# Optimization experiments

Hardware: AMD Instinct MI355X
Metric: run time of the kernel (lower is better)

## Reference

```python
import jax, jax.numpy as jnp
import numpy as np

V, D, H, L, RATIO, T_MAX = 1024, 512, 8, 11, 3, 1024
DH = D // H
HID = D * RATIO
NB, DB = 2048, 128  # bigram buckets / dim
EPS = 1e-6


def _rope_tables(T):
    pos = jnp.arange(T, dtype=jnp.float32)
    freqs = 1.0 / (10000.0 ** (jnp.arange(0, DH, 2, dtype=jnp.float32) / DH))
    emb = jnp.outer(pos, freqs)  # [T, DH/2]
    return jnp.cos(emb), jnp.sin(emb)


def _rmsnorm(x, w):
    return x * jax.lax.rsqrt(jnp.mean(x * x, axis=-1, keepdims=True) + EPS) * w


def setup_inputs() -> dict:
    key = jax.random.key(0)
    ks = jax.random.split(key, 10)
    B, T = 8, 1024
    s = 0.02
    return {
        "x": jax.random.randint(ks[0], (B, T), 0, V),
        "embed": jax.random.normal(ks[1], (V, D), jnp.float32) * s,
        "Wqkv": jax.random.normal(ks[2], (L, 3 * D, D), jnp.float32) * s,
        "Wproj": jax.random.normal(ks[3], (L, D, D), jnp.float32) * s,
        "n1_w": jnp.ones((L, D), jnp.float32),
        "n2_w": jnp.ones((L, D), jnp.float32),
        "Wfc1": jax.random.normal(ks[4], (L, HID, D), jnp.float32) * s,
        "Wfc2": jax.random.normal(ks[5], (L, D, HID), jnp.float32) * s,
        "norm_f_w": jnp.ones((D,), jnp.float32),
        "bg_embed": jax.random.normal(ks[6], (NB, DB), jnp.float32) * s,
        "bg_proj": jax.random.normal(ks[7], (V, DB), jnp.float32) * s,
    }


def _attn(x, Wqkv, Wproj, cos, sin, causal):
    B, T, C = x.shape
    qkv = x @ Wqkv.T  # [B,T,3D]
    q, k, v = jnp.split(qkv, 3, axis=-1)
    def heads(t):
        return t.reshape(B, T, H, DH).transpose(0, 2, 1, 3)  # [B,H,T,DH]
    q, k, v = heads(q), heads(k), heads(v)
    c = cos[None, None]  # [1,1,T,DH/2]
    s = sin[None, None]
    def rope(t):
        t1, t2 = t[..., : DH // 2], t[..., DH // 2 :]
        return jnp.concatenate([t1 * c - t2 * s, t1 * s + t2 * c], axis=-1)
    q, k = rope(q), rope(k)
    w = jnp.einsum("bhqd,bhkd->bhqk", q, k) * (DH ** -0.5)
    w = jnp.where(causal, w, -jnp.inf)
    w = jax.nn.softmax(w.astype(jnp.float32), axis=-1).astype(x.dtype)
    out = jnp.einsum("bhqk,bhkd->bhqd", w, v)
    self_w = jnp.diagonal(w, axis1=-2, axis2=-1)[..., None]  # [B,H,T,1]
    out = out - self_w * v  # XSA: subtract self-value contribution
    out = out.transpose(0, 2, 1, 3).reshape(B, T, C)
    return out @ Wproj.T


def reference(x, embed, Wqkv, Wproj, n1_w, n2_w, Wfc1, Wfc2, norm_f_w, bg_embed, bg_proj):
    B, T = x.shape
    cos, sin = _rope_tables(T_MAX)
    cos, sin = cos[:T], sin[:T]
    causal = jnp.tril(jnp.ones((T, T), dtype=bool))
    # bigram logits from previous token
    prev = jnp.concatenate([jnp.zeros((B, 1), x.dtype), x[:, :-1]], axis=1)
    bigram_logits = bg_embed[prev % NB] @ bg_proj.T  # [B,T,V]
    h = embed[x]
    for i in range(L):
        h = h + _attn(_rmsnorm(h, n1_w[i]), Wqkv[i], Wproj[i], cos, sin, causal)
        z = _rmsnorm(h, n2_w[i])
        h = h + jnp.square(jax.nn.relu(z @ Wfc1[i].T)) @ Wfc2[i].T
    h = _rmsnorm(h, norm_f_w)
    return h @ embed.T + bigram_logits
```

## Files before the change

### kernel.cpp

```cpp
#include <hip/hip_runtime.h>

#define NROW   8192
#define DMODEL 512
#define TSEQ   1024
#define LAYERS 11
#define HIDDEN 1536

typedef __bf16 bf16_t;
typedef bf16_t bf16x8 __attribute__((ext_vector_type(8)));
typedef bf16_t bf16x4 __attribute__((ext_vector_type(4)));
typedef float  f32x4  __attribute__((ext_vector_type(4)));
typedef unsigned int u32;
typedef u32 u32x4 __attribute__((ext_vector_type(4)));

#define GLD16(gp, lp) __builtin_amdgcn_global_load_lds( \
    (const __attribute__((address_space(1))) void*)(gp), \
    (__attribute__((address_space(3))) void*)(lp), 16, 0, 0)

#if __has_builtin(__builtin_amdgcn_exp2f)
#define EXP2(x) __builtin_amdgcn_exp2f(x)
#else
#define EXP2(x) exp2f(x)
#endif

__global__ void rope_table_k(float* __restrict__ cosT, float* __restrict__ sinT) {
    int i = blockIdx.x * blockDim.x + threadIdx.x;
    int t = i >> 5, j = i & 31;
    float freq = powf(10000.f, -(float)j * (1.f / 32.f));
    float ang = (float)t * freq;
    cosT[i] = cosf(ang);
    sinT[i] = sinf(ang);
}

__global__ void embed_gather_k(const int* __restrict__ x,
                               const float* __restrict__ embed,
                               float* __restrict__ h,
                               bf16_t* __restrict__ hb) {
    int n = blockIdx.x;
    int d = threadIdx.x;
    float4 v = ((const float4*)(embed + (size_t)x[n] * DMODEL))[d];
    ((float4*)(h + (size_t)n * DMODEL))[d] = v;
    bf16x4 o;
    o[0] = (bf16_t)v.x; o[1] = (bf16_t)v.y; o[2] = (bf16_t)v.z; o[3] = (bf16_t)v.w;
    *(bf16x4*)(hb + (size_t)n * DMODEL + d * 4) = o;
}

__global__ void bg_gather_k(const int* __restrict__ x,
                            const float* __restrict__ bge,
                            bf16_t* __restrict__ Afu) {
    int n = blockIdx.x;
    int t = n & (TSEQ - 1);
    int prev = (t == 0) ? 0 : x[n - 1];
    Afu[(size_t)n * 640 + 512 + threadIdx.x] = (bf16_t)bge[(size_t)prev * 128 + threadIdx.x];
}

__global__ void cvt_bf16_k(const float* __restrict__ in, bf16_t* __restrict__ out, int n8) {
    int i = blockIdx.x * blockDim.x + threadIdx.x;
    if (i >= n8) return;
    float4 a = ((const float4*)in)[2 * i];
    float4 b = ((const float4*)in)[2 * i + 1];
    bf16x8 o;
    o[0] = (bf16_t)a.x; o[1] = (bf16_t)a.y; o[2] = (bf16_t)a.z; o[3] = (bf16_t)a.w;
    o[4] = (bf16_t)b.x; o[5] = (bf16_t)b.y; o[6] = (bf16_t)b.z; o[7] = (bf16_t)b.w;
    ((bf16x8*)out)[i] = o;
}

__global__ void cvt_fold_k(const float* __restrict__ in,
                           const float* __restrict__ nw,
                           bf16_t* __restrict__ out, int n8, int layerSz) {
    int i = blockIdx.x * blockDim.x + threadIdx.x;
    if (i >= n8) return;
    int i8 = i * 8;
    int k = i8 & 511;
    int l = i8 / layerSz;
    const float* wv = nw + l * DMODEL + k;
    float4 a = ((const float4*)in)[2 * i];
    float4 b = ((const float4*)in)[2 * i + 1];
    float4 wa = *(const float4*)wv;
    float4 wb = *(const float4*)(wv + 4);
    bf16x8 o;
    o[0] = (bf16_t)(a.x * wa.x); o[1] = (bf16_t)(a.y * wa.y);
    o[2] = (bf16_t)(a.z * wa.z); o[3] = (bf16_t)(a.w * wa.w);
    o[4] = (bf16_t)(b.x * wb.x); o[5] = (bf16_t)(b.y * wb.y);
    o[6] = (bf16_t)(b.z * wb.z); o[7] = (bf16_t)(b.w * wb.w);
    ((bf16x8*)out)[i] = o;
}

__global__ void cvt_pad_k(const float* __restrict__ in, bf16_t* __restrict__ out,
                          int n8, int lshift, int mask, int colOff) {
    int i = blockIdx.x * blockDim.x + threadIdx.x;
    if (i >= n8) return;
    int i8 = i * 8;
    int row = i8 >> lshift;
    int col = i8 & mask;
    float4 a = ((const float4*)in)[2 * i];
    float4 b = ((const float4*)in)[2 * i + 1];
    bf16x8 o;
    o[0] = (bf16_t)a.x; o[1] = (bf16_t)a.y; o[2] = (bf16_t)a.z; o[3] = (bf16_t)a.w;
    o[4] = (bf16_t)b.x; o[5] = (bf16_t)b.y; o[6] = (bf16_t)b.z; o[7] = (bf16_t)b.w;
    *(bf16x8*)&out[(size_t)row * 640 + colOff + col] = o;
}

__global__ __launch_bounds__(256) void rmsnorm_k(const float* __restrict__ in,
                                                 const float* __restrict__ w,
                                                 bf16_t* __restrict__ out,
                                                 int ostride) {
    int wv = threadIdx.x >> 6, lane = threadIdx.x & 63;
    int row = (blockIdx.x << 2) + wv;
    const float* rp = in + (size_t)row * DMODEL + lane * 8;
    float4 v0 = *(const float4*)(rp);
    float4 v1 = *(const float4*)(rp + 4);
    float ss = v0.x*v0.x + v0.y*v0.y + v0.z*v0.z + v0.w*v0.w
             + v1.x*v1.x + v1.y*v1.y + v1.z*v1.z + v1.w*v1.w;
#pragma unroll
    for (int off = 32; off; off >>= 1) ss += __shfl_xor(ss, off, 64);
    float sc = rsqrtf(ss * (1.f / DMODEL) + 1e-6f);
    const float* wp = w + lane * 8;
    float4 w0 = *(const float4*)(wp);
    float4 w1 = *(const float4*)(wp + 4);
    bf16x8 o;
    o[0] = (bf16_t)(v0.x * sc * w0.x); o[1] = (bf16_t)(v0.y * sc * w0.y);
    o[2] = (bf16_t)(v0.z * sc * w0.z); o[3] = (bf16_t)(v0.w * sc * w0.w);
    o[4] = (bf16_t)(v1.x * sc * w1.x); o[5] = (bf16_t)(v1.y * sc * w1.y);
    o[6] = (bf16_t)(v1.z * sc * w1.z); o[7] = (bf16_t)(v1.w * sc * w1.w);
    *(bf16x8*)(out + (size_t)row * ostride + lane * 8) = o;
}

template<int BM, int EPI>
__global__ __launch_bounds__(256, 2)
void gemm_mfma(const bf16_t* __restrict__ A,
               const bf16_t* __restrict__ B,
               float* __restrict__ Cf,
               bf16_t* __restrict__ Cb,
               const float* __restrict__ cosT,
               const float* __restrict__ sinT,
               int M, int N, int K, int nbx) {
    constexpr int NT  = 256;
    constexpr int WM  = 2;
    constexpr int MI  = BM / WM / 16;
    constexpr int ACH = (BM * 4) / NT;
    constexpr int BCH = 2;
    constexpr int NBUF = (BM == 64) ? 4 : 3;
    constexpr bool SCALED = (EPI == 2 || EPI == 4);
    __shared__ __align__(16) bf16_t As[NBUF][BM * 32];
    __shared__ __align__(16) bf16_t Bs[NBUF][128 * 32];
    const int tid = threadIdx.x;
    const int w = tid >> 6, lane = tid & 63;

    const int nwg = (int)gridDim.x;
    const int bid = blockIdx.x;
    const int swz = (bid & 7) * (nwg >> 3) + (bid >> 3);
    const int bx = swz % nbx, by = swz / nbx;

    const int m0 = by * BM, n0 = bx * 128;
    const int wr = (w >> 1) * (BM / WM), wc = (w & 1) * 64;
    const int fr = lane & 15, fq = lane >> 4;

    f32x4 acc[MI][4] = {};
    float ssq[SCALED ? MI : 1] = {};

    float cold[EPI == 1 ? MI : 1][4][4];
    if constexpr (EPI == 1) {
#pragma unroll
        for (int i = 0; i < MI; ++i)
#pragma unroll
            for (int j = 0; j < 4; ++j)
#pragma unroll
                for (int q = 0; q < 4; ++q)
                    cold[i][j][q] = Cf[(size_t)(m0 + wr + i * 16 + fq * 4 + q) * N
                                       + n0 + wc + j * 16 + fr];
    }

    auto stage = [&](int k0, int buf) {
#pragma unroll
        for (int c = 0; c < ACH; ++c) {
            int idx = c * NT + tid;
            int row = idx >> 2, cs = idx & 3;
            GLD16(A + (size_t)(m0 + row) * K + k0 + cs * 8,
                  &As[buf][(size_t)(c * NT + w * 64) * 8]);
        }
#pragma unroll
        for (int c = 0; c < BCH; ++c) {
            int idx = c * NT + tid;
            int row = idx >> 2, cs = idx & 3;
            GLD16(B + (size_t)(n0 + row) * K + k0 + cs * 8,
                  &Bs[buf][(size_t)(c * NT + w * 64) * 8]);
        }
    };

    const int NK = K >> 5;
    stage(0, 0);
    stage(32, 1);
    for (int k = 0; k < NK; ++k) {
        const int cur = k % NBUF;
        if (k + 2 < NK) {
            stage((k + 2) << 5, (k + 2) % NBUF);
            if constexpr (BM == 128) asm volatile("s_waitcnt vmcnt(8)" ::: "memory");
            else                     asm volatile("s_waitcnt vmcnt(6)" ::: "memory");
        } else if (k + 1 < NK) {
            if constexpr (BM == 128) asm volatile("s_waitcnt vmcnt(4)" ::: "memory");
            else                     asm volatile("s_waitcnt vmcnt(3)" ::: "memory");
        } else {
            asm volatile("s_waitcnt vmcnt(0)" ::: "memory");
        }
        __builtin_amdgcn_s_barrier();
        __builtin_amdgcn_sched_barrier(0);

        bf16x8 a[MI], b[4];
        const bf16_t* ap = &As[cur][(size_t)(wr + fr) * 32 + fq * 8];
        const bf16_t* bp = &Bs[cur][(size_t)(wc + fr) * 32 + fq * 8];
#pragma unroll
        for (int i = 0; i < MI; ++i) a[i] = *(const bf16x8*)(ap + i * 16 * 32);
#pragma unroll
        for (int j = 0; j < 4; ++j)  b[j] = *(const bf16x8*)(bp + j * 16 * 32);
        __builtin_amdgcn_s_setprio(1);
#pragma unroll
        for (int i = 0; i < MI; ++i)
#pragma unroll
            for (int j = 0; j < 4; ++j)
                acc[i][j] = __builtin_amdgcn_mfma_f32_16x16x32_bf16(a[i], b[j], acc[i][j], 0, 0, 0);
        __builtin_amdgcn_s_setprio(0);

        if constexpr (SCALED) {
#pragma unroll
            for (int i = 0; i < MI; ++i)
#pragma unroll
                for (int j = 0; j < 8; ++j) {
                    float f = (float)a[i][j];
                    ssq[i] = fmaf(f, f, ssq[i]);
                }
        }

        if constexpr (NBUF == 3) {
            asm volatile("s_waitcnt lgkmcnt(0)" ::: "memory");
            __builtin_amdgcn_s_barrier();
            __builtin_amdgcn_sched_barrier(0);
        }
    }

    float sld[SCALED ? MI : 1][4];
    if constexpr (SCALED) {
#pragma unroll
        for (int i = 0; i < MI; ++i) {
            ssq[i] += __shfl_xor(ssq[i], 16, 64);
            ssq[i] += __shfl_xor(ssq[i], 32, 64);
#pragma unroll
            for (int q = 0; q < 4; ++q) {
                float v = __shfl(ssq[i], fq * 4 + q, 64);
                sld[i][q] = rsqrtf(v * (1.f / DMODEL) + 1e-6f);
            }
        }
    }

    if (EPI == 4) {
        const bool qk = (n0 + wc) < 1024;
#pragma unroll
        for (int i = 0; i < MI; ++i) {
#pragma unroll
            for (int q = 0; q < 4; ++q) {
                int row = m0 + wr + i * 16 + fq * 4 + q;
                size_t rb = (size_t)row * N + n0 + wc;
                float sm = sld[i][q];
                if (qk) {
                    int t = row & (TSEQ - 1);
#pragma unroll
                    for (int j = 0; j < 2; ++j) {
                        int d = j * 16 + fr;
                        float c = cosT[t * 32 + d];
                        float s = sinT[t * 32 + d];
                        float v1 = acc[i][j][q] * sm, v2 = acc[i][j + 2][q] * sm;
                        Cb[rb + j * 16 + fr]       = (bf16_t)(v1 * c - v2 * s);
                        Cb[rb + (j + 2) * 16 + fr] = (bf16_t)(v1 * s + v2 * c);
                    }
                } else {
#pragma unroll
                    for (int j = 0; j < 4; ++j)
                        Cb[rb + j * 16 + fr] = (bf16_t)(acc[i][j][q] * sm);
                }
            }
        }
        return;
    }
#pragma unroll
    for (int i = 0; i < MI; ++i) {
        int row = m0 + wr + i * 16 + fq * 4;
#pragma unroll
        for (int j = 0; j < 4; ++j) {
            int col = n0 + wc + j * 16 + fr;
#pragma unroll
            for (int q = 0; q < 4; ++q) {
                float v = acc[i][j][q];
                size_t off = (size_t)(row + q) * N + col;
                if (EPI == 0)      Cf[off] = v;
                else if (EPI == 1) {
                    float nv = cold[i][j][q] + v;
                    Cf[off] = nv;
                    Cb[off] = (bf16_t)nv;
                } else if (EPI == 2) {
                    v = fmaxf(v * sld[i][q], 0.f);
                    Cb[off] = (bf16_t)(v * v);
                }
            }
        }
    }
}

__global__ __launch_bounds__(512) void attn_mfma_k(const bf16_t* __restrict__ qkvb,
                                                   bf16_t* __restrict__ outb) {
    __shared__ __align__(16) bf16_t Ks[2][64 * 64];
    __shared__ __align__(16) bf16_t VsT[2][2 * 64 * 32];

    const int tid = threadIdx.x;
    const int w  = tid >> 6;
    const int ln = tid & 63;
    const int lr = ln & 15;
    const int lg = ln >> 4;

    const int bid = blockIdx.x;
    const int p  = 7 - (bid >> 6);
    const int bh = bid & 63;
    const int b = bh >> 3, h = bh & 7;
    const int lastT = (p << 7) + 64;
    const int tq0  = (p << 7) + w * 16;
    const int qrow = tq0 + lr;
    const int wlast = tq0 & ~63;

    const bf16_t* Qg = qkvb + (size_t)b * TSEQ * 1536 + h * 64;
    const bf16_t* Kg = Qg + 512;
    const bf16_t* Vg = Qg + 1024;

    const int mk = tid >> 4;
    const int md = tid & 15;
    const int src0 = lr + 32 * (lg & 1);
    const int fsel = lg >> 1;
    const int gofs = 8 * (lg ^ ((lr >> 2) & 3));

    auto KSTAGE = [&](int t0, int buf) {
        int key = w * 8 + (ln >> 3);
        int dc  = (ln & 7) ^ (ln >> 3);
        GLD16(Kg + (size_t)(t0 + key) * 1536 + dc * 8, &Ks[buf][w * 512]);
    };
    auto VLOAD = [&](int t0, bf16x4* rv) {
#pragma unroll
        for (int i = 0; i < 4; ++i)
            rv[i] = *(const bf16x4*)(Vg + (size_t)(t0 + mk * 4 + i) * 1536 + md * 4);
    };
    auto VWRITE = [&](const bf16x4* rv, int buf) {
        const int s = mk >> 3;
#pragma unroll
        for (int jj = 0; jj < 4; ++jj) {
            int row = md * 4 + jj;
            bf16x4 wv;
            wv[0] = rv[0][jj]; wv[1] = rv[1][jj]; wv[2] = rv[2][jj]; wv[3] = rv[3][jj];
            int gx = (mk & 7) ^ ((md & 3) << 1);
            *(bf16x4*)&VsT[buf][s * 2048 + row * 32 + gx * 4] = wv;
        }
    };

    bf16x8 qreg[2];
    {
        const float QS = 0.1803368801f;
        const bf16_t* qp = Qg + (size_t)qrow * 1536 + lg * 8;
        qreg[0] = *(const bf16x8*)qp;
        qreg[1] = *(const bf16x8*)(qp + 32);
#pragma unroll
        for (int jj = 0; jj < 8; ++jj) {
            qreg[0][jj] = (bf16_t)((float)qreg[0][jj] * QS);
            qreg[1][jj] = (bf16_t)((float)qreg[1][jj] * QS);
        }
    }

    f32x4 accO[4] = {};
    float mrun = -1e30f, pl = 0.f, esf = 0.f;

    {
        bf16x4 rv[4];
        KSTAGE(0, 0);
        if (w < 4) VLOAD(0, rv);
        asm volatile("s_waitcnt vmcnt(0)" ::: "memory");
        if (w < 4) VWRITE(rv, 0);
        asm volatile("s_waitcnt lgkmcnt(0)" ::: "memory");
        __builtin_amdgcn_s_barrier();
        __builtin_amdgcn_sched_barrier(0);
    }

    for (int t0 = 0; t0 <= lastT; t0 += 64) {
        const int cur = (t0 >> 6) & 1;
        const bool more = t0 < lastT;
        bf16x4 rv[4];
        if (more) {
            KSTAGE(t0 + 64, cur ^ 1);
            if (w < 4) VLOAD(t0 + 64, rv);
        }

        if (t0 <= wlast) {
            const bool masked = t0 == wlast;

            f32x4 sq[4] = {};
            __builtin_amdgcn_s_setprio(1);
#pragma unroll
            for (int kr = 0; kr < 4; ++kr) {
                int key = kr * 16 + lr;
#pragma unroll
                for (int s = 0; s < 2; ++s) {
                    int chunk = key * 8 + ((s * 4 + lg) ^ (key & 7));
                    bf16x8 kf = *(const bf16x8*)&Ks[cur][chunk * 8];
                    sq[kr] = __builtin_amdgcn_mfma_f32_16x16x32_bf16(kf, qreg[s], sq[kr], 0, 0, 0);
                }
            }
            __builtin_amdgcn_s_setprio(0);

            float e16[4][4];
            float tm = -1e30f;
            if (masked) {
#pragma unroll
                for (int f = 0; f < 4; ++f)
#pragma unroll
                    for (int r = 0; r < 4; ++r) {
                        int key = t0 + f * 16 + lg * 4 + r;
                        float sv = (key <= qrow) ? sq[f][r] : -1e30f;
                        e16[f][r] = sv;
                        tm = fmaxf(tm, sv);
                    }
            } else {
#pragma unroll
                for (int f = 0; f < 4; ++f)
#pragma unroll
                    for (int r = 0; r < 4; ++r) {
                        e16[f][r] = sq[f][r];
                        tm = fmaxf(tm, sq[f][r]);
                    }
            }
            tm = fmaxf(tm, __shfl_xor(tm, 16, 64));
            tm = fmaxf(tm, __shfl_xor(tm, 32, 64));

            const bool resc = __any(tm > mrun + 8.f);
            float mnew = resc ? fmaxf(mrun, tm) : mrun;
            float psum = 0.f;
#pragma unroll
            for (int f = 0; f < 4; ++f)
#pragma unroll
                for (int r = 0; r < 4; ++r) {
                    float e = EXP2(e16[f][r] - mnew);
                    e16[f][r] = e;
                    psum += e;
                }
            float pd = 0.f;
            if (masked) {
#pragma unroll
                for (int f = 0; f < 4; ++f)
#pragma unroll
                    for (int r = 0; r < 4; ++r) {
                        int key = t0 + f * 16 + lg * 4 + r;
                        pd = (key == qrow) ? e16[f][r] : pd;
                    }
            }
            if (resc) {
                float corr = EXP2(mrun - mnew);
                mrun = mnew;
                pl  = pl  * corr + psum;
                esf = esf * corr + pd;
#pragma unroll
                for (int dblk = 0; dblk < 4; ++dblk)
#pragma unroll
                    for (int r = 0; r < 4; ++r) accO[dblk][r] *= corr;
            } else {
                pl  += psum;
                esf += pd;
            }

            u32 plo[4], phi[4];
#pragma unroll
            for (int f = 0; f < 4; ++f) {
                bf16x4 t;
                t[0] = (bf16_t)e16[f][0]; t[1] = (bf16_t)e16[f][1];
                t[2] = (bf16_t)e16[f][2]; t[3] = (bf16_t)e16[f][3];
                uint2 pr = __builtin_bit_cast(uint2, t);
                plo[f] = pr.x; phi[f] = pr.y;
            }

#pragma unroll
            for (int s = 0; s < 2; ++s) {
                u32 a0 = (u32)__shfl((int)plo[s * 2],     src0,      64);
                u32 a1 = (u32)__shfl((int)phi[s * 2],     src0,      64);
                u32 a2 = (u32)__shfl((int)plo[s * 2],     src0 + 16, 64);
                u32 a3 = (u32)__shfl((int)phi[s * 2],     src0 + 16, 64);
                u32 c0 = (u32)__shfl((int)plo[s * 2 + 1], src0,      64);
                u32 c1 = (u32)__shfl((int)phi[s * 2 + 1], src0,      64);
                u32 c2 = (u32)__shfl((int)plo[s * 2 + 1], src0 + 16, 64);
                u32 c3 = (u32)__shfl((int)phi[s * 2 + 1], src0 + 16, 64);
                u32x4 bw;
                bw[0] = fsel ? c0 : a0;
                bw[1] = fsel ? c1 : a1;
                bw[2] = fsel ? c2 : a2;
                bw[3] = fsel ? c3 : a3;
                bf16x8 bfrag = __builtin_bit_cast(bf16x8, bw);
                __builtin_amdgcn_s_setprio(1);
#pragma unroll
                for (int dblk = 0; dblk < 4; ++dblk) {
                    bf16x8 av = *(const bf16x8*)&VsT[cur][s * 2048 + (dblk * 16 + lr) * 32 + gofs];
                    accO[dblk] = __builtin_amdgcn_mfma_f32_16x16x32_bf16(av, bfrag, accO[dblk], 0, 0, 0);
                }
                __builtin_amdgcn_s_setprio(0);
            }
        }

        if (more) {
            asm volatile("s_waitcnt vmcnt(0)" ::: "memory");
            if (w < 4) VWRITE(rv, cur ^ 1);
            asm volatile("s_waitcnt lgkmcnt(0)" ::: "memory");
            __builtin_amdgcn_s_barrier();
            __builtin_amdgcn_sched_barrier(0);
        }
    }

    pl  += __shfl_xor(pl, 16, 64);  pl  += __shfl_xor(pl, 32, 64);
    esf += __shfl_xor(esf, 16, 64); esf += __shfl_xor(esf, 32, 64);
    float rin = 1.0f / pl;
    const bf16_t* vqp = Vg + (size_t)qrow * 1536;
    bf16_t* op = outb + (size_t)(b * TSEQ + qrow) * DMODEL + h * 64;
#pragma unroll
    for (int dblk = 0; dblk < 4; ++dblk) {
        bf16x4 vq = *(const bf16x4*)(vqp + dblk * 16 + lg * 4);
        bf16x4 o4;
#pragma unroll
        for (int r = 0; r < 4; ++r)
            o4[r] = (bf16_t)((accO[dblk][r] - esf * (float)vq[r]) * rin);
        *(bf16x4*)(op + dblk * 16 + lg * 4) = o4;
    }
}

static inline void cvt(const float* in, bf16_t* out, size_t n, hipStream_t s) {
    int n8 = (int)(n / 8);
    cvt_bf16_k<<<(n8 + 255) / 256, 256, 0, s>>>(in, out, n8);
}

extern "C" void kernel_launch(void* const* d_in, const int* in_sizes, int n_in,
                              void* d_out, int out_size, void* d_ws, size_t ws_size,
                              hipStream_t stream) {
    const int*   x     = (const int*)d_in[0];
    const float* embed = (const float*)d_in[1];
    const float* Wqkv  = (const float*)d_in[2];
    const float* Wproj = (const float*)d_in[3];
    const float* n1w   = (const float*)d_in[4];
    const float* n2w   = (const float*)d_in[5];
    const float* Wfc1  = (const float*)d_in[6];
    const float* Wfc2  = (const float*)d_in[7];
    const float* normf = (const float*)d_in[8];
    const float* bge   = (const float*)d_in[9];
    const float* bgp   = (const float*)d_in[10];
    float* out = (float*)d_out;

    float* ws   = (float*)d_ws;
    float* cosT = ws;
    float* sinT = cosT + 32768;
    float* h    = sinT + 32768;
    bf16_t* qkvb = (bf16_t*)(h + (size_t)NROW * DMODEL);
    bf16_t* ub   = qkvb;
    bf16_t* Afu  = qkvb;
    bf16_t* hb   = qkvb + (size_t)NROW * 1536;
    bf16_t* atb  = hb  + (size_t)NROW * DMODEL;
    bf16_t* wqb  = atb + (size_t)NROW * DMODEL;
    bf16_t* wpb  = wqb + (size_t)LAYERS * 3 * DMODEL * DMODEL;
    bf16_t* w1b  = wpb + (size_t)LAYERS * DMODEL * DMODEL;
    bf16_t* w2b  = w1b + (size_t)LAYERS * HIDDEN * DMODEL;
    bf16_t* bfu  = w2b + (size_t)LAYERS * DMODEL * HIDDEN;

    rope_table_k<<<128, 256, 0, stream>>>(cosT, sinT);
    embed_gather_k<<<NROW, 128, 0, stream>>>(x, embed, h, hb);

    {
        int n8q = (int)((size_t)LAYERS * 3 * DMODEL * DMODEL / 8);
        cvt_fold_k<<<(n8q + 255) / 256, 256, 0, stream>>>(Wqkv, n1w, wqb, n8q, 3 * DMODEL * DMODEL);
        int n81 = (int)((size_t)LAYERS * HIDDEN * DMODEL / 8);
        cvt_fold_k<<<(n81 + 255) / 256, 256, 0, stream>>>(Wfc1, n2w, w1b, n81, HIDDEN * DMODEL);
    }
    cvt(Wproj, wpb, (size_t)LAYERS * DMODEL * DMODEL, stream);
    cvt(Wfc2,  w2b, (size_t)LAYERS * DMODEL * HIDDEN, stream);
    cvt_pad_k<<<(65536 + 255) / 256, 256, 0, stream>>>(embed, bfu, 65536, 9, 511, 0);
    cvt_pad_k<<<(16384 + 255) / 256, 256, 0, stream>>>(bgp,   bfu, 16384, 7, 127, 512);

    for (int i = 0; i < LAYERS; ++i) {
        gemm_mfma<128, 4><<<768, 256, 0, stream>>>(
            hb, wqb + (size_t)i * 3 * DMODEL * DMODEL, nullptr, qkvb,
            cosT, sinT, NROW, 3 * DMODEL, DMODEL, 12);
        attn_mfma_k<<<512, 512, 0, stream>>>(qkvb, atb);
        gemm_mfma<64, 1><<<512, 256, 0, stream>>>(
            atb, wpb + (size_t)i * DMODEL * DMODEL, h, hb,
            nullptr, nullptr, NROW, DMODEL, DMODEL, 4);
        gemm_mfma<128, 2><<<768, 256, 0, stream>>>(
            hb, w1b + (size_t)i * HIDDEN * DMODEL, nullptr, ub,
            nullptr, nullptr, NROW, HIDDEN, DMODEL, 12);
        gemm_mfma<64, 1><<<512, 256, 0, stream>>>(
            ub, w2b + (size_t)i * DMODEL * HIDDEN, h, hb,
            nullptr, nullptr, NROW, DMODEL, HIDDEN, 4);
    }

    rmsnorm_k<<<NROW / 4, 256, 0, stream>>>(h, normf, Afu, 640);
    bg_gather_k<<<NROW, 128, 0, stream>>>(x, bge, Afu);
    gemm_mfma<128, 0><<<512, 256, 0, stream>>>(
        Afu, bfu, out, nullptr, nullptr, nullptr, NROW, 1024, 640, 8);
}
```

Measured before the change: 1.457 ms.

## Triple-buffer K/V tiles in attention with two-ahead prefetch and split V staging

The attention kernel moves from double to triple buffering of K and V tiles in LDS, issuing the loads for tile t+2 while computing tile t. It uses partial vmcnt waits so only the older tile's loads must land before the barrier. V staging now uses all 8 waves, each loading 2 rows instead of 4 waves loading 4 rows, and writes bf16x2 pairs into the transposed LDS layout. The aim is to hide global load latency behind compute, at the cost of more LDS (which may lower occupancy) and fragile hand-counted waitcnt values.

```diff
diff --git a/kernel.cpp b/kernel.cpp
--- a/kernel.cpp
+++ b/kernel.cpp
@@ -9,6 +9,7 @@
 typedef __bf16 bf16_t;
 typedef bf16_t bf16x8 __attribute__((ext_vector_type(8)));
 typedef bf16_t bf16x4 __attribute__((ext_vector_type(4)));
+typedef bf16_t bf16x2 __attribute__((ext_vector_type(2)));
 typedef float  f32x4  __attribute__((ext_vector_type(4)));
 typedef unsigned int u32;
 typedef u32 u32x4 __attribute__((ext_vector_type(4)));
@@ -307,8 +308,8 @@
 
 __global__ __launch_bounds__(512) void attn_mfma_k(const bf16_t* __restrict__ qkvb,
                                                    bf16_t* __restrict__ outb) {
-    __shared__ __align__(16) bf16_t Ks[2][64 * 64];
-    __shared__ __align__(16) bf16_t VsT[2][2 * 64 * 32];
+    __shared__ __align__(16) bf16_t Ks[3][64 * 64];
+    __shared__ __align__(16) bf16_t VsT[3][2 * 64 * 32];
 
     const int tid = threadIdx.x;
     const int w  = tid >> 6;
@@ -320,10 +321,10 @@
     const int p  = 7 - (bid >> 6);
     const int bh = bid & 63;
     const int b = bh >> 3, h = bh & 7;
-    const int lastT = (p << 7) + 64;
+    const int Tn = (p << 1) + 1;
     const int tq0  = (p << 7) + w * 16;
     const int qrow = tq0 + lr;
-    const int wlast = tq0 & ~63;
+    const int wlastIdx = (tq0 >> 6);
 
     const bf16_t* Qg = qkvb + (size_t)b * TSEQ * 1536 + h * 64;
     const bf16_t* Kg = Qg + 512;
@@ -335,25 +336,27 @@
     const int fsel = lg >> 1;
     const int gofs = 8 * (lg ^ ((lr >> 2) & 3));
 
-    auto KSTAGE = [&](int t0, int buf) {
+    auto KSTAGE = [&](int tI, int buf) {
         int key = w * 8 + (ln >> 3);
         int dc  = (ln & 7) ^ (ln >> 3);
-        GLD16(Kg + (size_t)(t0 + key) * 1536 + dc * 8, &Ks[buf][w * 512]);
+        GLD16(Kg + (size_t)(tI * 64 + key) * 1536 + dc * 8, &Ks[buf][w * 512]);
     };
-    auto VLOAD = [&](int t0, bf16x4* rv) {
-#pragma unroll
-        for (int i = 0; i < 4; ++i)
-            rv[i] = *(const bf16x4*)(Vg + (size_t)(t0 + mk * 4 + i) * 1536 + md * 4);
+    auto VLOAD = [&](int tI, bf16x4 (&rv)[2]) {
+#pragma unroll
+        for (int i = 0; i < 2; ++i)
+            rv[i] = *(const bf16x4*)(Vg + (size_t)(tI * 64 + 2 * mk + i) * 1536 + md * 4);
     };
-    auto VWRITE = [&](const bf16x4* rv, int buf) {
-        const int s = mk >> 3;
-#pragma unroll
-        for (int jj = 0; jj < 4; ++jj) {
-            int row = md * 4 + jj;
-            bf16x4 wv;
-            wv[0] = rv[0][jj]; wv[1] = rv[1][jj]; wv[2] = rv[2][jj]; wv[3] = rv[3][jj];
-            int gx = (mk & 7) ^ ((md & 3) << 1);
-            *(bf16x4*)&VsT[buf][s * 2048 + row * 32 + gx * 4] = wv;
+    auto VWRITE = [&](const bf16x4 (&rv)[2], int buf) {
+        const int sv = mk >> 4;
+        const int kp = mk & 15;
+        const int m4 = kp >> 1;
+        const int lo = kp & 1;
+#pragma unroll
+        for (int j = 0; j < 4; ++j) {
+            int row = md * 4 + j;
+            int gx  = m4 ^ ((md & 3) << 1);
+            bf16x2 wv; wv[0] = rv[0][j]; wv[1] = rv[1][j];
+            *(bf16x2*)&VsT[buf][sv * 2048 + row * 32 + gx * 4 + lo * 2] = wv;
         }
     };
 
@@ -373,145 +376,146 @@
     f32x4 accO[4] = {};
     float mrun = -1e30f, pl = 0.f, esf = 0.f;
 
-    {
-        bf16x4 rv[4];
-        KSTAGE(0, 0);
-        if (w < 4) VLOAD(0, rv);
-        asm volatile("s_waitcnt vmcnt(0)" ::: "memory");
-        if (w < 4) VWRITE(rv, 0);
-        asm volatile("s_waitcnt lgkmcnt(0)" ::: "memory");
-        __builtin_amdgcn_s_barrier();
-        __builtin_amdgcn_sched_barrier(0);
-    }
-
-    for (int t0 = 0; t0 <= lastT; t0 += 64) {
-        const int cur = (t0 >> 6) & 1;
-        const bool more = t0 < lastT;
-        bf16x4 rv[4];
-        if (more) {
-            KSTAGE(t0 + 64, cur ^ 1);
-            if (w < 4) VLOAD(t0 + 64, rv);
-        }
-
-        if (t0 <= wlast) {
-            const bool masked = t0 == wlast;
-
-            f32x4 sq[4] = {};
+    auto TILE = [&](int t, int bc, bool masked) {
+        const int t0 = t * 64;
+        f32x4 sq[4] = {};
+        __builtin_amdgcn_s_setprio(1);
+#pragma unroll
+        for (int kr = 0; kr < 4; ++kr) {
+            int key = kr * 16 + lr;
+#pragma unroll
+            for (int s = 0; s < 2; ++s) {
+                int chunk = key * 8 + ((s * 4 + lg) ^ (key & 7));
+                bf16x8 kf = *(const bf16x8*)&Ks[bc][chunk * 8];
+                sq[kr] = __builtin_amdgcn_mfma_f32_16x16x32_bf16(kf, qreg[s], sq[kr], 0, 0, 0);
+            }
+        }
+        __builtin_amdgcn_s_setprio(0);
+
+        float e16[4][4];
+        float tm = -1e30f;
+        if (masked) {
+#pragma unroll
+            for (int f = 0; f < 4; ++f)
+#pragma unroll
+                for (int r = 0; r < 4; ++r) {
+                    int key = t0 + f * 16 + lg * 4 + r;
+                    float sv = (key <= qrow) ? sq[f][r] : -1e30f;
+                    e16[f][r] = sv;
+                    tm = fmaxf(tm, sv);
+                }
+        } else {
+#pragma unroll
+            for (int f = 0; f < 4; ++f)
+#pragma unroll
+                for (int r = 0; r < 4; ++r) {
+                    e16[f][r] = sq[f][r];
+                    tm = fmaxf(tm, sq[f][r]);
+                }
+        }
+        tm = fmaxf(tm, __shfl_xor(tm, 16, 64));
+        tm = fmaxf(tm, __shfl_xor(tm, 32, 64));
+
+        const bool resc = __any(tm > mrun + 8.f);
+        float mnew = resc ? fmaxf(mrun, tm) : mrun;
+        float psum = 0.f;
+#pragma unroll
+        for (int f = 0; f < 4; ++f)
+#pragma unroll
+            for (int r = 0; r < 4; ++r) {
+                float e = EXP2(e16[f][r] - mnew);
+                e16[f][r] = e;
+                psum += e;
+            }
+        float pd = 0.f;
+        if (masked) {
+#pragma unroll
+            for (int f = 0; f < 4; ++f)
+#pragma unroll
+                for (int r = 0; r < 4; ++r) {
+                    int key = t0 + f * 16 + lg * 4 + r;
+                    pd = (key == qrow) ? e16[f][r] : pd;
+                }
+        }
+        if (resc) {
+            float corr = EXP2(mrun - mnew);
+            mrun = mnew;
+            pl  = pl  * corr + psum;
+            esf = esf * corr + pd;
+#pragma unroll
+            for (int dblk = 0; dblk < 4; ++dblk)
+#pragma unroll
+                for (int r = 0; r < 4; ++r) accO[dblk][r] *= corr;
+        } else {
+            pl  += psum;
+            esf += pd;
+        }
+
+        u32 plo[4], phi[4];
+#pragma unroll
+        for (int f = 0; f < 4; ++f) {
+            bf16x4 tt;
+            tt[0] = (bf16_t)e16[f][0]; tt[1] = (bf16_t)e16[f][1];
+            tt[2] = (bf16_t)e16[f][2]; tt[3] = (bf16_t)e16[f][3];
+            uint2 pr = __builtin_bit_cast(uint2, tt);
+            plo[f] = pr.x; phi[f] = pr.y;
+        }
+
+#pragma unroll
+        for (int s = 0; s < 2; ++s) {
+            u32 a0 = (u32)__shfl((int)plo[s * 2],     src0,      64);
+            u32 a1 = (u32)__shfl((int)phi[s * 2],     src0,      64);
+            u32 a2 = (u32)__shfl((int)plo[s * 2],     src0 + 16, 64);
+            u32 a3 = (u32)__shfl((int)phi[s * 2],     src0 + 16, 64);
+            u32 c0 = (u32)__shfl((int)plo[s * 2 + 1], src0,      64);
+            u32 c1 = (u32)__shfl((int)phi[s * 2 + 1], src0,      64);
+            u32 c2 = (u32)__shfl((int)plo[s * 2 + 1], src0 + 16, 64);
+            u32 c3 = (u32)__shfl((int)phi[s * 2 + 1], src0 + 16, 64);
+            u32x4 bw;
+            bw[0] = fsel ? c0 : a0;
+            bw[1] = fsel ? c1 : a1;
+            bw[2] = fsel ? c2 : a2;
+            bw[3] = fsel ? c3 : a3;
+            bf16x8 bfrag = __builtin_bit_cast(bf16x8, bw);
             __builtin_amdgcn_s_setprio(1);
 #pragma unroll
-            for (int kr = 0; kr < 4; ++kr) {
-                int key = kr * 16 + lr;
-#pragma unroll
-                for (int s = 0; s < 2; ++s) {
-                    int chunk = key * 8 + ((s * 4 + lg) ^ (key & 7));
-                    bf16x8 kf = *(const bf16x8*)&Ks[cur][chunk * 8];
-                    sq[kr] = __builtin_amdgcn_mfma_f32_16x16x32_bf16(kf, qreg[s], sq[kr], 0, 0, 0);
-                }
+            for (int dblk = 0; dblk < 4; ++dblk) {
+                bf16x8 av = *(const bf16x8*)&VsT[bc][s * 2048 + (dblk * 16 + lr) * 32 + gofs];
+                accO[dblk] = __builtin_amdgcn_mfma_f32_16x16x32_bf16(av, bfrag, accO[dblk], 0, 0, 0);
             }
             __builtin_amdgcn_s_setprio(0);
-
-            float e16[4][4];
-            float tm = -1e30f;
-            if (masked) {
-#pragma unroll
-                for (int f = 0; f < 4; ++f)
-#pragma unroll
-                    for (int r = 0; r < 4; ++r) {
-                        int key = t0 + f * 16 + lg * 4 + r;
-                        float sv = (key <= qrow) ? sq[f][r] : -1e30f;
-                        e16[f][r] = sv;
-                        tm = fmaxf(tm, sv);
-                    }
-            } else {
-#pragma unroll
-                for (int f = 0; f < 4; ++f)
-#pragma unroll
-                    for (int r = 0; r < 4; ++r) {
-                        e16[f][r] = sq[f][r];
-                        tm = fmaxf(tm, sq[f][r]);
-                    }
-            }
-            tm = fmaxf(tm, __shfl_xor(tm, 16, 64));
-            tm = fmaxf(tm, __shfl_xor(tm, 32, 64));
-
-            const bool resc = __any(tm > mrun + 8.f);
-            float mnew = resc ? fmaxf(mrun, tm) : mrun;
-            float psum = 0.f;
-#pragma unroll
-            for (int f = 0; f < 4; ++f)
-#pragma unroll
-                for (int r = 0; r < 4; ++r) {
-                    float e = EXP2(e16[f][r] - mnew);
-                    e16[f][r] = e;
-                    psum += e;
-                }
-            float pd = 0.f;
-            if (masked) {
-#pragma unroll
-                for (int f = 0; f < 4; ++f)
-#pragma unroll
-                    for (int r = 0; r < 4; ++r) {
-                        int key = t0 + f * 16 + lg * 4 + r;
-                        pd = (key == qrow) ? e16[f][r] : pd;
-                    }
-            }
-            if (resc) {
-                float corr = EXP2(mrun - mnew);
-                mrun = mnew;
-                pl  = pl  * corr + psum;
-                esf = esf * corr + pd;
-#pragma unroll
-                for (int dblk = 0; dblk < 4; ++dblk)
-#pragma unroll
-                    for (int r = 0; r < 4; ++r) accO[dblk][r] *= corr;
-            } else {
-                pl  += psum;
-                esf += pd;
-            }
-
-            u32 plo[4], phi[4];
-#pragma unroll
-            for (int f = 0; f < 4; ++f) {
-                bf16x4 t;
-                t[0] = (bf16_t)e16[f][0]; t[1] = (bf16_t)e16[f][1];
-                t[2] = (bf16_t)e16[f][2]; t[3] = (bf16_t)e16[f][3];
-                uint2 pr = __builtin_bit_cast(uint2, t);
-                plo[f] = pr.x; phi[f] = pr.y;
-            }
-
-#pragma unroll
-            for (int s = 0; s < 2; ++s) {
-                u32 a0 = (u32)__shfl((int)plo[s * 2],     src0,      64);
-                u32 a1 = (u32)__shfl((int)phi[s * 2],     src0,      64);
-                u32 a2 = (u32)__shfl((int)plo[s * 2],     src0 + 16, 64);
-                u32 a3 = (u32)__shfl((int)phi[s * 2],     src0 + 16, 64);
-                u32 c0 = (u32)__shfl((int)plo[s * 2 + 1], src0,      64);
-                u32 c1 = (u32)__shfl((int)phi[s * 2 + 1], src0,      64);
-                u32 c2 = (u32)__shfl((int)plo[s * 2 + 1], src0 + 16, 64);
-                u32 c3 = (u32)__shfl((int)phi[s * 2 + 1], src0 + 16, 64);
-                u32x4 bw;
-                bw[0] = fsel ? c0 : a0;
-                bw[1] = fsel ? c1 : a1;
-                bw[2] = fsel ? c2 : a2;
-                bw[3] = fsel ? c3 : a3;
-                bf16x8 bfrag = __builtin_bit_cast(bf16x8, bw);
-                __builtin_amdgcn_s_setprio(1);
-#pragma unroll
-                for (int dblk = 0; dblk < 4; ++dblk) {
-                    bf16x8 av = *(const bf16x8*)&VsT[cur][s * 2048 + (dblk * 16 + lr) * 32 + gofs];
-                    accO[dblk] = __builtin_amdgcn_mfma_f32_16x16x32_bf16(av, bfrag, accO[dblk], 0, 0, 0);
-                }
-                __builtin_amdgcn_s_setprio(0);
-            }
-        }
-
-        if (more) {
-            asm volatile("s_waitcnt vmcnt(0)" ::: "memory");
-            if (w < 4) VWRITE(rv, cur ^ 1);
+        }
+    };
+
+    bf16x4 rvA[2], rvB[2];
+
+    KSTAGE(0, 0); VLOAD(0, rvB);
+    KSTAGE(1, 1); VLOAD(1, rvA);
+    asm volatile("s_waitcnt vmcnt(3)" ::: "memory");
+    VWRITE(rvB, 0);
+    asm volatile("s_waitcnt lgkmcnt(0)" ::: "memory");
+    __builtin_amdgcn_s_barrier();
+    __builtin_amdgcn_sched_barrier(0);
+
+    int bc = 0, bn = 1, bs2 = 2;
+    auto BODY = [&](int t, bf16x4 (&rvLand)[2], bf16x4 (&rvIssue)[2]) {
+        const bool issue = (t + 2 <= Tn);
+        if (issue) { KSTAGE(t + 2, bs2); VLOAD(t + 2, rvIssue); }
+        if (t <= wlastIdx) TILE(t, bc, t == wlastIdx);
+        if (t + 1 <= Tn) {
+            if (issue) asm volatile("s_waitcnt vmcnt(3)" ::: "memory");
+            else       asm volatile("s_waitcnt vmcnt(0)" ::: "memory");
+            VWRITE(rvLand, bn);
             asm volatile("s_waitcnt lgkmcnt(0)" ::: "memory");
             __builtin_amdgcn_s_barrier();
             __builtin_amdgcn_sched_barrier(0);
         }
+        int tmp = bc; bc = bn; bn = bs2; bs2 = tmp;
+    };
+
+    for (int t = 0; t <= Tn; t += 2) {
+        BODY(t,     rvA, rvB);
+        BODY(t + 1, rvB, rvA);
     }
 
     pl  += __shfl_xor(pl, 16, 64);  pl  += __shfl_xor(pl, 32, 64);
```

Result: no change. 1.465 ms (+0.5%).
